# Kernel tuning notes

Measured on AMD Instinct MI355X. Metric: run time of the kernel, lower is better.

The kernel has to match this reference:

```python
import jax, jax.numpy as jnp
import numpy as np

B, L, D_MODEL = 8, 2048, 512
N_QUBITS, Q_LAYERS = 10, 4
DIM = 2 ** N_QUBITS
EPS = 1e-5  # torch LayerNorm default


def _apply_1q_tok(state, U, q):
    # per-token 2x2 gate U: (N,2,2), wire 0 = most significant (PennyLane order)
    N = state.shape[0]
    s = state.reshape(N, 2 ** q, 2, -1)
    return jnp.einsum('nij,najb->naib', U, s).reshape(N, -1)


def _apply_1q(state, U, q):
    # shared 2x2 gate U: (2,2)
    N = state.shape[0]
    s = state.reshape(N, 2 ** q, 2, -1)
    return jnp.einsum('ij,najb->naib', U, s).reshape(N, -1)


def _cnot(state, c, t):
    N = state.shape[0]
    lo, hi = min(c, t), max(c, t)
    s = state.reshape(N, 2 ** lo, 2, 2 ** (hi - lo - 1), 2, -1)
    if c < t:
        # control is the first 2-axis; flip target axis where control==1
        s = s.at[:, :, 1].set(jnp.flip(s[:, :, 1], axis=3))
    else:
        # target is the first 2-axis, control the second
        s = s.at[:, :, :, :, 1].set(jnp.flip(s[:, :, :, :, 1], axis=2))
    return s.reshape(N, -1)


def _simulate(feats, weights):
    # feats: (N, n_qubits) angles; weights: (q_layers, n_qubits, 2)
    N = feats.shape[0]
    half = 0.5 * feats
    cxa = jnp.cos(half).astype(jnp.complex64)
    sxa = jnp.sin(half).astype(jnp.complex64)
    phz = jnp.exp(1j * half.astype(jnp.complex64))  # e^{+i theta/2}
    state = jnp.zeros((N, DIM), jnp.complex64).at[:, 0].set(1.0 + 0j)
    for l in range(Q_LAYERS):
        # AngleEmbedding rotation='X' : RX(feat_q) on wire q
        for q in range(N_QUBITS):
            c, s = cxa[:, q], sxa[:, q]
            U = jnp.stack([jnp.stack([c, -1j * s], -1),
                           jnp.stack([-1j * s, c], -1)], -2)  # (N,2,2)
            state = _apply_1q_tok(state, U, q)
        # AngleEmbedding rotation='Z' : RZ(feat_q) on wire q (diagonal)
        for q in range(N_QUBITS):
            p = phz[:, q]
            diag = jnp.stack([jnp.conj(p), p], -1)  # (N,2)
            s = state.reshape(N, 2 ** q, 2, -1)
            state = (s * diag[:, None, :, None]).reshape(N, -1)
        # trainable RY, RZ per wire (shared across tokens)
        for q in range(N_QUBITS):
            ty = 0.5 * weights[l, q, 0]
            cy, sy = jnp.cos(ty), jnp.sin(ty)
            Uy = jnp.stack([jnp.stack([cy, -sy]), jnp.stack([sy, cy])]).astype(jnp.complex64)
            state = _apply_1q(state, Uy, q)
            pz = jnp.exp(1j * (0.5 * weights[l, q, 1]).astype(jnp.complex64))
            diag = jnp.stack([jnp.conj(pz), pz])  # (2,)
            s = state.reshape(N, 2 ** q, 2, -1)
            state = (s * diag[None, None, :, None]).reshape(N, -1)
        # entangling CNOT ring
        for q in range(N_QUBITS):
            state = _cnot(state, q, (q + 1) % N_QUBITS)
    probs = jnp.real(state) ** 2 + jnp.imag(state) ** 2  # (N, 2**n)
    zs = []
    for q in range(N_QUBITS):
        p = probs.reshape(N, 2 ** q, 2, -1).sum(axis=(1, 3))  # (N,2)
        zs.append(p[:, 0] - p[:, 1])  # <Z_q>
    return jnp.stack(zs, -1)  # (N, n_qubits)


def setup_inputs() -> dict:
    key = jax.random.key(0)
    ks = jax.random.split(key, 4)
    x = jax.random.normal(ks[0], (B, L, D_MODEL), jnp.float32)
    in_W = jax.random.normal(ks[1], (N_QUBITS, D_MODEL), jnp.float32) / np.float32(np.sqrt(D_MODEL))
    in_b = jnp.zeros((N_QUBITS,), jnp.float32)
    gamma = jnp.ones((N_QUBITS,), jnp.float32)
    beta = jnp.zeros((N_QUBITS,), jnp.float32)
    weights = 0.05 * jax.random.normal(ks[2], (Q_LAYERS, N_QUBITS, 2), jnp.float32)
    out_W = jax.random.normal(ks[3], (D_MODEL, N_QUBITS), jnp.float32) / np.float32(np.sqrt(N_QUBITS))
    out_b = jnp.zeros((D_MODEL,), jnp.float32)
    return {"x": x, "in_W": in_W, "in_b": in_b, "gamma": gamma, "beta": beta,
            "weights": weights, "out_W": out_W, "out_b": out_b}


def reference(x, in_W, in_b, gamma, beta, weights, out_W, out_b):
    Bs, Ls, _ = x.shape
    h = jnp.tanh(jnp.einsum('bld,qd->blq', x, in_W) + in_b)
    mu = h.mean(-1, keepdims=True)
    var = ((h - mu) ** 2).mean(-1, keepdims=True)
    h = (h - mu) / jnp.sqrt(var + EPS) * gamma + beta
    q_out = _simulate(h.reshape(Bs * Ls, N_QUBITS), weights)
    q_out = q_out.reshape(Bs, Ls, N_QUBITS).astype(x.dtype)
    return x + jnp.einsum('blq,dq->bld', q_out, out_W) + out_b
```

## Files before the change

### kernel.cpp

```cpp
#include <hip/hip_runtime.h>

#define NQ 10
#define DQ 512
#define QL 4
#define NTOK (8 * 2048)

typedef float v2f __attribute__((ext_vector_type(2)));
typedef float v4f __attribute__((ext_vector_type(4)));

template <int CTRL>
__device__ __forceinline__ float dppf(float v) {
    int i = __builtin_bit_cast(int, v);
    i = __builtin_amdgcn_update_dpp(i, i, CTRL, 0xF, 0xF, false);
    return __builtin_bit_cast(float, i);
}
template <int M>
__device__ __forceinline__ float lx(float v) {
    if constexpr (M == 1)      return dppf<0xB1>(v);
    else if constexpr (M == 2) return dppf<0x4E>(v);
    else if constexpr (M == 8) return dppf<0x128>(v);
    else return __shfl_xor(v, M);
}
template <int M>
__device__ __forceinline__ v2f lx2(v2f v) {
    v2f r; r.x = lx<M>(v.x); r.y = lx<M>(v.y); return r;
}

__device__ __forceinline__ void reduce10(float* z) {
#pragma unroll
    for (int q = 0; q < NQ; ++q) {
        z[q] += lx<32>(z[q]); z[q] += lx<16>(z[q]); z[q] += lx<8>(z[q]);
        z[q] += lx<4>(z[q]);  z[q] += lx<2>(z[q]);  z[q] += lx<1>(z[q]);
    }
}

__device__ __forceinline__ v4f coef(const v4f* Q, float c, float s) {
    float A = c * c, C = c * s;
    return Q[0] + A * Q[1] + C * Q[2];
}

template <int M>
__device__ __forceinline__ void gate_lane(v2f* sr2, v2f* si2, v4f cf, bool bit) {
    const float ar = cf.x;
    const float Ai = bit ? -cf.y : cf.y;
    const float Br = bit ? cf.z : -cf.z;
    const float bi = cf.w;
#pragma unroll
    for (int j = 0; j < 8; ++j) {
        v2f wr = lx2<M>(sr2[j]), wi = lx2<M>(si2[j]);
        v2f nr = ar * sr2[j] - Ai * si2[j] + Br * wr - bi * wi;
        v2f ni = ar * si2[j] + Ai * sr2[j] + Br * wi + bi * wr;
        sr2[j] = nr; si2[j] = ni;
    }
}
template <int BJ>
__device__ __forceinline__ void gate_reg(v2f* sr2, v2f* si2, v4f cf) {
    const float ar = cf.x, ai = cf.y, br = cf.z, bi = cf.w;
#pragma unroll
    for (int j = 0; j < 8; ++j) if (!(j & BJ)) {
        const int j1 = j | BJ;
        v2f x0r = sr2[j], x0i = si2[j], x1r = sr2[j1], x1i = si2[j1];
        sr2[j]  = ar * x0r - ai * x0i - br * x1r - bi * x1i;
        si2[j]  = ar * x0i + ai * x0r - br * x1i + bi * x1r;
        sr2[j1] = br * x0r - bi * x0i + ar * x1r + ai * x1i;
        si2[j1] = br * x0i + bi * x0r + ar * x1i - ai * x1r;
    }
}
__device__ __forceinline__ void gate_elem(v2f* sr2, v2f* si2, v4f cf) {
    const float ar = cf.x, ai = cf.y, br = cf.z, bi = cf.w;
    const v2f cA = {ar, br}, cB = {-ai, -bi}, cC = {-br, ar}, cD = {-bi, ai};
    const v2f cF = {ai, bi}, cH = {bi, -ai};
#pragma unroll
    for (int j = 0; j < 8; ++j) {
        float x0r = sr2[j].x, x0i = si2[j].x, x1r = sr2[j].y, x1i = si2[j].y;
        v2f nr = x0r * cA + x0i * cB + x1r * cC + x1i * cD;
        v2f ni = x0i * cA + x0r * cF + x1i * cC + x1r * cH;
        sr2[j] = nr; si2[j] = ni;
    }
}

__device__ __forceinline__ void perm678(v2f* a) {
    float t;
    t = a[1].x; a[1].x = a[1].y; a[1].y = t;
    t = a[2].x; a[2].x = a[3].x; a[3].x = a[2].y; a[2].y = a[3].y; a[3].y = t;
    t = a[4].x; a[4].x = a[6].x; a[6].x = a[5].x; a[5].x = a[7].y; a[7].y = t;
    t = a[4].y; a[4].y = a[6].y; a[6].y = a[5].y; a[5].y = a[7].x; a[7].x = t;
}

__device__ __forceinline__ void cnot_ring(v2f* sr2, v2f* si2, int lane, int srcl) {
#pragma unroll
    for (int j = 0; j < 8; ++j) {
        sr2[j].x = __shfl(sr2[j].x, srcl); sr2[j].y = __shfl(sr2[j].y, srcl);
        si2[j].x = __shfl(si2[j].x, srcl); si2[j].y = __shfl(si2[j].y, srcl);
    }
    {
        const bool ctrl = (lane & 1);
#pragma unroll
        for (int j = 0; j < 4; ++j) {
            v2f t0 = sr2[j], t1 = sr2[j + 4];
            sr2[j]     = ctrl ? t1 : t0;
            sr2[j + 4] = ctrl ? t0 : t1;
            t0 = si2[j]; t1 = si2[j + 4];
            si2[j]     = ctrl ? t1 : t0;
            si2[j + 4] = ctrl ? t0 : t1;
        }
    }
    perm678(sr2);
    perm678(si2);
#pragma unroll
    for (int j = 0; j < 8; ++j) {
        sr2[j].y = __shfl_xor(sr2[j].y, 32);
        si2[j].y = __shfl_xor(si2[j].y, 32);
    }
}

__global__ __launch_bounds__(256) void quantum_kernel(
    const float* __restrict__ x, const float* __restrict__ in_W,
    const float* __restrict__ in_b, const float* __restrict__ gamma,
    const float* __restrict__ beta, const float* __restrict__ weights,
    const float* __restrict__ out_W, const float* __restrict__ out_b,
    float* __restrict__ out)
{
    __shared__ v2f lds_oW2[NQ * (DQ / 2)];
    __shared__ v4f ldsQ[QL * NQ * 3];
    float* lds_f = (float*)lds_oW2;
    const int t = threadIdx.x;
#pragma unroll
    for (int rep = 0; rep < 2; ++rep) {
        const int d = t + rep * 256;
#pragma unroll
        for (int q = 0; q < NQ; ++q)
            lds_f[q * DQ + d] = out_W[d * NQ + q];
    }
    if (t < QL * NQ) {
        float w0 = weights[t * 2], w1 = weights[t * 2 + 1];
        float cy = __cosf(0.5f * w0), sy = __sinf(0.5f * w0);
        float cz = __cosf(0.5f * w1), sz = __sinf(0.5f * w1);
        float d = cy - sy, e = cy + sy;
        ldsQ[t * 3 + 0] = (v4f){-cz * sy,  sz * sy,  cz * cy,  sz * cy};
        ldsQ[t * 3 + 1] = (v4f){ cz * e,  -sz * e,  -cz * d,  -sz * d};
        ldsQ[t * 3 + 2] = (v4f){-sz * d,  -cz * d,   sz * e,  -cz * e};
    }
    __syncthreads();

    const int lane = t & 63;
    const int tok = blockIdx.x * 4 + (t >> 6);

    int srcl = lane;
#pragma unroll
    for (int q = 4; q >= 0; --q) {
        const int bc = 5 - q, bt = bc - 1;
        srcl ^= ((srcl >> bc) & 1) << bt;
    }

    const v2f* xrow2 = (const v2f*)(x + (size_t)tok * DQ);
    const v2f* inW2 = (const v2f*)in_W;
    v2f hv[NQ];
#pragma unroll
    for (int q = 0; q < NQ; ++q) hv[q] = (v2f){0.f, 0.f};
#pragma unroll
    for (int k = 0; k < 4; ++k) {
        v2f xk = xrow2[lane + 64 * k];
#pragma unroll
        for (int q = 0; q < NQ; ++q)
            hv[q] = xk * inW2[q * (DQ / 2) + lane + 64 * k] + hv[q];
    }
    float h[NQ];
#pragma unroll
    for (int q = 0; q < NQ; ++q) h[q] = hv[q].x + hv[q].y;
    reduce10(h);

    float mu = 0.f;
#pragma unroll
    for (int q = 0; q < NQ; ++q) {
        float e = __expf(2.f * (h[q] + in_b[q]));
        h[q] = (e - 1.f) * __builtin_amdgcn_rcpf(e + 1.f);
        mu += h[q];
    }
    mu *= 0.1f;
    float var = 0.f;
#pragma unroll
    for (int q = 0; q < NQ; ++q) { float d0 = h[q] - mu; var += d0 * d0; }
    var *= 0.1f;
    const float rstd = rsqrtf(var + 1e-5f);

    float cq[NQ], sq[NQ];
#pragma unroll
    for (int q = 0; q < NQ; ++q) {
        float f = (h[q] - mu) * rstd * gamma[q] + beta[q];
        float hf = 0.5f * f;
        cq[q] = __cosf(hf);
        sq[q] = __sinf(hf);
    }

    v2f sr2[8], si2[8];
    {
        const v4f* Q0 = &ldsQ[0];
        v4f f0 = coef(Q0 + 0, cq[0], sq[0]);
        bool b0 = (lane & 32);
        float Lr = b0 ? f0.z : f0.x, Li = b0 ? f0.w : f0.y;
#pragma unroll
        for (int q = 1; q < 6; ++q) {
            v4f f = coef(Q0 + 3 * q, cq[q], sq[q]);
            bool b = lane & (1 << (5 - q));
            float fr = b ? f.z : f.x, fi = b ? f.w : f.y;
            float nr = Lr * fr - Li * fi, ni = Lr * fi + Li * fr;
            Lr = nr; Li = ni;
        }
        float Pr[8], Pi[8];
        {
            v4f f6 = coef(Q0 + 18, cq[6], sq[6]);
            Pr[0] = Lr * f6.x - Li * f6.y; Pi[0] = Lr * f6.y + Li * f6.x;
            Pr[4] = Lr * f6.z - Li * f6.w; Pi[4] = Lr * f6.w + Li * f6.z;
        }
        {
            v4f f7 = coef(Q0 + 21, cq[7], sq[7]);
#pragma unroll
            for (int jj = 0; jj < 8; jj += 4) {
                float tr1 = Pr[jj] * f7.z - Pi[jj] * f7.w;
                float ti1 = Pr[jj] * f7.w + Pi[jj] * f7.z;
                float tr0 = Pr[jj] * f7.x - Pi[jj] * f7.y;
                float ti0 = Pr[jj] * f7.y + Pi[jj] * f7.x;
                Pr[jj] = tr0; Pi[jj] = ti0; Pr[jj + 2] = tr1; Pi[jj + 2] = ti1;
            }
        }
        {
            v4f f8 = coef(Q0 + 24, cq[8], sq[8]);
#pragma unroll
            for (int jj = 0; jj < 8; jj += 2) {
                float tr1 = Pr[jj] * f8.z - Pi[jj] * f8.w;
                float ti1 = Pr[jj] * f8.w + Pi[jj] * f8.z;
                float tr0 = Pr[jj] * f8.x - Pi[jj] * f8.y;
                float ti0 = Pr[jj] * f8.y + Pi[jj] * f8.x;
                Pr[jj] = tr0; Pi[jj] = ti0; Pr[jj + 1] = tr1; Pi[jj + 1] = ti1;
            }
        }
        {
            v4f f9 = coef(Q0 + 27, cq[9], sq[9]);
            v2f c9r = {f9.x, f9.z}, c9i = {f9.y, f9.w};
#pragma unroll
            for (int j = 0; j < 8; ++j) {
                sr2[j] = Pr[j] * c9r - Pi[j] * c9i;
                si2[j] = Pr[j] * c9i + Pi[j] * c9r;
            }
        }
    }
    cnot_ring(sr2, si2, lane, srcl);

#pragma unroll 1
    for (int l = 1; l < QL; ++l) {
        const v4f* Ql = &ldsQ[l * NQ * 3];
        gate_lane<32>(sr2, si2, coef(Ql + 0,  cq[0], sq[0]), lane & 32);
        gate_lane< 8>(sr2, si2, coef(Ql + 6,  cq[2], sq[2]), lane & 8);
        gate_lane<16>(sr2, si2, coef(Ql + 3,  cq[1], sq[1]), lane & 16);
        gate_lane< 2>(sr2, si2, coef(Ql + 12, cq[4], sq[4]), lane & 2);
        gate_lane< 4>(sr2, si2, coef(Ql + 9,  cq[3], sq[3]), lane & 4);
        gate_lane< 1>(sr2, si2, coef(Ql + 15, cq[5], sq[5]), lane & 1);
        gate_reg<4>(sr2, si2, coef(Ql + 18, cq[6], sq[6]));
        gate_reg<2>(sr2, si2, coef(Ql + 21, cq[7], sq[7]));
        gate_reg<1>(sr2, si2, coef(Ql + 24, cq[8], sq[8]));
        gate_elem(sr2, si2, coef(Ql + 27, cq[9], sq[9]));
        cnot_ring(sr2, si2, lane, srcl);
    }

    v2f aP = {0.f, 0.f}, a6 = {0.f, 0.f}, a7 = {0.f, 0.f}, a8 = {0.f, 0.f};
#pragma unroll
    for (int j = 0; j < 8; ++j) {
        v2f p = sr2[j] * sr2[j] + si2[j] * si2[j];
        aP += p;
        if (j & 4) a6 -= p; else a6 += p;
        if (j & 2) a7 -= p; else a7 += p;
        if (j & 1) a8 -= p; else a8 += p;
    }
    const float P = aP.x + aP.y;
    float z[NQ];
#pragma unroll
    for (int q = 0; q < 6; ++q)
        z[q] = (lane & (1 << (5 - q))) ? -P : P;
    z[6] = a6.x + a6.y; z[7] = a7.x + a7.y; z[8] = a8.x + a8.y;
    z[9] = aP.x - aP.y;
    reduce10(z);

    v2f* orow2 = (v2f*)(out + (size_t)tok * DQ);
    const v2f* ob2 = (const v2f*)out_b;
#pragma unroll
    for (int k = 0; k < 4; ++k) {
        const int d2 = lane + 64 * k;
        v2f acc = xrow2[d2] + ob2[d2];
#pragma unroll
        for (int q = 0; q < NQ; ++q)
            acc = z[q] * lds_oW2[q * (DQ / 2) + d2] + acc;
        orow2[d2] = acc;
    }
}

extern "C" void kernel_launch(void* const* d_in, const int* in_sizes, int n_in,
                              void* d_out, int out_size, void* d_ws, size_t ws_size,
                              hipStream_t stream) {
    const float* x       = (const float*)d_in[0];
    const float* in_W    = (const float*)d_in[1];
    const float* in_b    = (const float*)d_in[2];
    const float* gamma   = (const float*)d_in[3];
    const float* beta    = (const float*)d_in[4];
    const float* weights = (const float*)d_in[5];
    const float* out_W   = (const float*)d_in[6];
    const float* out_b   = (const float*)d_in[7];
    float* out = (float*)d_out;

    dim3 grid(NTOK / 4), block(256);
    hipLaunchKernelGGL(quantum_kernel, grid, block, 0, stream,
                       x, in_W, in_b, gamma, beta, weights, out_W, out_b, out);
}
```

Baseline: 231.0 us.

## Move per-block out_W transpose and gate coefficients into a one-shot prep kernel

Adds a single-block prep kernel that transposes out_W and precomputes the per-layer gate coefficient table into workspace memory once per call. The main kernel then reads these from global memory (through cache) instead of every block rebuilding them in LDS and running a __syncthreads. This removes redundant per-block setup work and LDS use, which may raise occupancy. The cost is an extra kernel launch, and coefficient and out_W reads in the hot loops now go through global memory and cache instead of LDS.

```diff
diff --git a/kernel.cpp b/kernel.cpp
--- a/kernel.cpp
+++ b/kernel.cpp
@@ -4,6 +4,7 @@
 #define DQ 512
 #define QL 4
 #define NTOK (8 * 2048)
+#define QOFF (NQ * DQ)
 
 typedef float v2f __attribute__((ext_vector_type(2)));
 typedef float v4f __attribute__((ext_vector_type(4)));
@@ -114,37 +115,36 @@
     }
 }
 
-__global__ __launch_bounds__(256) void quantum_kernel(
-    const float* __restrict__ x, const float* __restrict__ in_W,
-    const float* __restrict__ in_b, const float* __restrict__ gamma,
-    const float* __restrict__ beta, const float* __restrict__ weights,
-    const float* __restrict__ out_W, const float* __restrict__ out_b,
-    float* __restrict__ out)
+__global__ __launch_bounds__(512) void prep_kernel(
+    const float* __restrict__ weights, const float* __restrict__ out_W,
+    float* __restrict__ ws)
 {
-    __shared__ v2f lds_oW2[NQ * (DQ / 2)];
-    __shared__ v4f ldsQ[QL * NQ * 3];
-    float* lds_f = (float*)lds_oW2;
     const int t = threadIdx.x;
 #pragma unroll
-    for (int rep = 0; rep < 2; ++rep) {
-        const int d = t + rep * 256;
-#pragma unroll
-        for (int q = 0; q < NQ; ++q)
-            lds_f[q * DQ + d] = out_W[d * NQ + q];
-    }
+    for (int q = 0; q < NQ; ++q)
+        ws[q * DQ + t] = out_W[t * NQ + q];
     if (t < QL * NQ) {
         float w0 = weights[t * 2], w1 = weights[t * 2 + 1];
         float cy = __cosf(0.5f * w0), sy = __sinf(0.5f * w0);
         float cz = __cosf(0.5f * w1), sz = __sinf(0.5f * w1);
         float d = cy - sy, e = cy + sy;
-        ldsQ[t * 3 + 0] = (v4f){-cz * sy,  sz * sy,  cz * cy,  sz * cy};
-        ldsQ[t * 3 + 1] = (v4f){ cz * e,  -sz * e,  -cz * d,  -sz * d};
-        ldsQ[t * 3 + 2] = (v4f){-sz * d,  -cz * d,   sz * e,  -cz * e};
-    }
-    __syncthreads();
-
+        v4f* Q = (v4f*)(ws + QOFF);
+        Q[t * 3 + 0] = (v4f){-cz * sy,  sz * sy,  cz * cy,  sz * cy};
+        Q[t * 3 + 1] = (v4f){ cz * e,  -sz * e,  -cz * d,  -sz * d};
+        Q[t * 3 + 2] = (v4f){-sz * d,  -cz * d,   sz * e,  -cz * e};
+    }
+}
+
+__global__ __launch_bounds__(256) void quantum_kernel(
+    const float* __restrict__ x, const float* __restrict__ in_W,
+    const float* __restrict__ in_b, const float* __restrict__ gamma,
+    const float* __restrict__ beta, const float* __restrict__ ws,
+    const float* __restrict__ out_b, float* __restrict__ out)
+{
+    const int t = threadIdx.x;
     const int lane = t & 63;
     const int tok = blockIdx.x * 4 + (t >> 6);
+    const v4f* Qg = (const v4f*)(ws + QOFF);
 
     int srcl = lane;
 #pragma unroll
@@ -195,7 +195,7 @@
 
     v2f sr2[8], si2[8];
     {
-        const v4f* Q0 = &ldsQ[0];
+        const v4f* Q0 = Qg;
         v4f f0 = coef(Q0 + 0, cq[0], sq[0]);
         bool b0 = (lane & 32);
         float Lr = b0 ? f0.z : f0.x, Li = b0 ? f0.w : f0.y;
@@ -249,7 +249,7 @@
 
 #pragma unroll 1
     for (int l = 1; l < QL; ++l) {
-        const v4f* Ql = &ldsQ[l * NQ * 3];
+        const v4f* Ql = Qg + l * NQ * 3;
         gate_lane<32>(sr2, si2, coef(Ql + 0,  cq[0], sq[0]), lane & 32);
         gate_lane< 8>(sr2, si2, coef(Ql + 6,  cq[2], sq[2]), lane & 8);
         gate_lane<16>(sr2, si2, coef(Ql + 3,  cq[1], sq[1]), lane & 16);
@@ -283,13 +283,14 @@
 
     v2f* orow2 = (v2f*)(out + (size_t)tok * DQ);
     const v2f* ob2 = (const v2f*)out_b;
+    const v2f* oWt2 = (const v2f*)ws;
 #pragma unroll
     for (int k = 0; k < 4; ++k) {
         const int d2 = lane + 64 * k;
         v2f acc = xrow2[d2] + ob2[d2];
 #pragma unroll
         for (int q = 0; q < NQ; ++q)
-            acc = z[q] * lds_oW2[q * (DQ / 2) + d2] + acc;
+            acc = z[q] * oWt2[q * (DQ / 2) + d2] + acc;
         orow2[d2] = acc;
     }
 }
@@ -306,8 +307,10 @@
     const float* out_W   = (const float*)d_in[6];
     const float* out_b   = (const float*)d_in[7];
     float* out = (float*)d_out;
-
-    dim3 grid(NTOK / 4), block(256);
-    hipLaunchKernelGGL(quantum_kernel, grid, block, 0, stream,
-                       x, in_W, in_b, gamma, beta, weights, out_W, out_b, out);
-}
+    float* ws = (float*)d_ws;
+
+    hipLaunchKernelGGL(prep_kernel, dim3(1), dim3(512), 0, stream,
+                       weights, out_W, ws);
+    hipLaunchKernelGGL(quantum_kernel, dim3(NTOK / 4), dim3(256), 0, stream,
+                       x, in_W, in_b, gamma, beta, ws, out_b, out);
+}
```

After: 234.2 us. No clear change (+1.4%).
